# Kernel optimization log

Hardware: AMD Instinct MI355X
Metric: run time of the kernel (lower is better)

## Reference

```python
import jax, jax.numpy as jnp
import numpy as np

NUM_NODES = 50000
NUM_EDGES = 640000
IN_FEAT = 128
OUT_FEAT = 128


def setup_inputs() -> dict:
    key = jax.random.key(0)
    k1, k2, k3, k4 = jax.random.split(key, 4)
    features = jax.random.normal(k1, (NUM_NODES, IN_FEAT), dtype=jnp.float32)
    weight = jax.random.normal(k2, (IN_FEAT, OUT_FEAT), dtype=jnp.float32) * (1.0 / np.sqrt(IN_FEAT))
    edges_dst = jax.random.randint(k3, (NUM_EDGES,), 0, NUM_NODES, dtype=jnp.int32)
    edges_src = jax.random.randint(k4, (NUM_EDGES,), 0, NUM_NODES, dtype=jnp.int32)
    return {"features": features, "weight": weight, "edges_dst": edges_dst, "edges_src": edges_src}


def reference(features, weight, edges_dst, edges_src):
    # nodes_representation = features @ W   -> [N, out_feat]
    nodes_representation = jnp.matmul(features, weight)

    # gather neighbor (source) features: [E, in_feat]
    neighbour = features[edges_src]

    # unsorted_segment_mean over target node ids (edges_dst)
    seg_sum = jax.ops.segment_sum(neighbour, edges_dst, num_segments=NUM_NODES)
    counts = jax.ops.segment_sum(jnp.ones((NUM_EDGES,), dtype=features.dtype),
                                 edges_dst, num_segments=NUM_NODES)
    aggregated = jnp.where(counts[:, None] > 0, seg_sum / jnp.maximum(counts[:, None], 1.0), 0.0)

    aggregated_messages = jnp.matmul(aggregated, weight)  # [N, out_feat]

    # combination_type == 'concat', activation == 'relu'
    h = jnp.concatenate([nodes_representation, aggregated_messages], axis=-1)  # [N, 2*out_feat]
    return jax.nn.relu(h)
```

## Files before the change

### kernel.cpp

```cpp
#include <hip/hip_runtime.h>

#define FEAT 128
#define NPB 50
#define NB 1000
#define MAGIC50 85899346u
#define CELL 16
#define CAP 48
#define SBLK 256
#define SB_STRIDE 136

typedef __attribute__((ext_vector_type(8))) short bhalf8;
typedef __attribute__((ext_vector_type(4))) float floatx4;

__device__ __forceinline__ unsigned int cvtpk(float lo, float hi) {
    unsigned int r;
    asm("v_cvt_pk_bf16_f32 %0, %1, %2" : "=v"(r) : "v"(lo), "v"(hi));
    return r;
}

__device__ __forceinline__ void acc8(float* a, uint4 v) {
    a[0] += __uint_as_float(v.x << 16);
    a[1] += __uint_as_float(v.x & 0xffff0000u);
    a[2] += __uint_as_float(v.y << 16);
    a[3] += __uint_as_float(v.y & 0xffff0000u);
    a[4] += __uint_as_float(v.z << 16);
    a[5] += __uint_as_float(v.z & 0xffff0000u);
    a[6] += __uint_as_float(v.w << 16);
    a[7] += __uint_as_float(v.w & 0xffff0000u);
}

__global__ __launch_bounds__(256, 2) void fused_kernel(
    const float* __restrict__ feat, const float* __restrict__ W,
    unsigned short* __restrict__ P2, float* __restrict__ out, int nrows,
    const int* __restrict__ edst, const int* __restrict__ esrc,
    unsigned int* __restrict__ binned, int nE)
{
    __shared__ __align__(16) char smem[NB * CELL * 4 + (NB / 4) * 4];

    const int tid = threadIdx.x;

    if (blockIdx.x < SBLK) {
        unsigned int* lbin  = (unsigned int*)smem;
        unsigned int* cur32 = (unsigned int*)(smem + NB * CELL * 4);

        const int blk = blockIdx.x;
        for (int i = tid; i < NB / 4; i += 256) cur32[i] = 0u;
        __syncthreads();

        const int nE4 = nE >> 2;
        const int perBlk = (nE4 + SBLK - 1) / SBLK;
        const int gBeg = blk * perBlk;
        const int gEnd = min(gBeg + perBlk, nE4);

        for (int g = gBeg + tid; g < gEnd; g += 256) {
            int4 d = *(const int4*)&edst[g << 2];
            int4 s = *(const int4*)&esrc[g << 2];
            #pragma unroll
            for (int e = 0; e < 4; ++e) {
                int dd = (e == 0) ? d.x : (e == 1) ? d.y : (e == 2) ? d.z : d.w;
                int ss = (e == 0) ? s.x : (e == 1) ? s.y : (e == 2) ? s.z : s.w;
                unsigned int bin = __umulhi((unsigned int)dd, MAGIC50);
                int local = dd - (int)bin * NPB;
                const int sh = (bin & 3) * 8;
                unsigned int old = atomicAdd(&cur32[bin >> 2], 1u << sh);
                int slot = (int)((old >> sh) & 0xffu);
                if (slot < CELL - 1)
                    lbin[bin * CELL + 1 + slot] =
                        ((unsigned int)local << 16) | (unsigned int)(ss & 0xffff);
            }
        }
        if (blk == 0) {
            for (int i = (nE4 << 2) + tid; i < nE; i += 256) {
                int dd = edst[i], ss = esrc[i];
                unsigned int bin = __umulhi((unsigned int)dd, MAGIC50);
                int local = dd - (int)bin * NPB;
                const int sh = (bin & 3) * 8;
                unsigned int old = atomicAdd(&cur32[bin >> 2], 1u << sh);
                int slot = (int)((old >> sh) & 0xffu);
                if (slot < CELL - 1)
                    lbin[bin * CELL + 1 + slot] =
                        ((unsigned int)local << 16) | (unsigned int)(ss & 0xffff);
            }
        }
        __syncthreads();

        for (int bin = tid; bin < NB; bin += 256) {
            unsigned int c = (cur32[bin >> 2] >> ((bin & 3) * 8)) & 0xffu;
            lbin[bin * CELL] = min(c, (unsigned int)(CELL - 1));
        }
        __syncthreads();

        const int lane = tid & 63;
        const int wv   = tid >> 6;
        const int q    = lane & 3;
        for (int cg = wv * 16 + (lane >> 2); cg < NB; cg += 64) {
            uint4 v = *(const uint4*)&lbin[cg * CELL + q * 4];
            *(uint4*)&binned[((size_t)cg * SBLK + blk) * CELL + q * 4] = v;
        }
        return;
    }

    unsigned short* sB = (unsigned short*)smem;
    const int bx   = blockIdx.x - SBLK;
    const int wave = tid >> 6;
    const int lane = tid & 63;
    const int m    = lane & 15;
    const int kg   = lane >> 4;

    for (int i = tid; i < 2048; i += 256) {
        int n  = i & 127;
        int kc = i >> 7;
        const float* wp = &W[(size_t)(kc * 8) * FEAT + n];
        float f[8];
        #pragma unroll
        for (int t = 0; t < 8; ++t) f[t] = wp[(size_t)t * FEAT];
        uint4 p;
        p.x = cvtpk(f[0], f[1]);
        p.y = cvtpk(f[2], f[3]);
        p.z = cvtpk(f[4], f[5]);
        p.w = cvtpk(f[6], f[7]);
        *(uint4*)&sB[n * SB_STRIDE + kc * 8] = p;
    }

    const int row  = bx * 64 + wave * 16 + m;
    const int rowc = min(row, nrows - 1);
    bhalf8 afrag[4];
    {
        const float* ap = &feat[(size_t)rowc * FEAT + kg * 8];
        #pragma unroll
        for (int ks = 0; ks < 4; ++ks) {
            float4 f0 = *(const float4*)&ap[ks * 32];
            float4 f1 = *(const float4*)&ap[ks * 32 + 4];
            union { bhalf8 v; unsigned int u[4]; } a;
            a.u[0] = cvtpk(f0.x, f0.y);
            a.u[1] = cvtpk(f0.z, f0.w);
            a.u[2] = cvtpk(f1.x, f1.y);
            a.u[3] = cvtpk(f1.z, f1.w);
            afrag[ks] = a.v;
        }
    }

    __syncthreads();

    floatx4 acc[8];
    #pragma unroll
    for (int nt = 0; nt < 8; ++nt) acc[nt] = (floatx4){0.f, 0.f, 0.f, 0.f};

    #pragma unroll
    for (int ks = 0; ks < 4; ++ks) {
        #pragma unroll
        for (int nt = 0; nt < 8; ++nt) {
            bhalf8 b = *(bhalf8*)&sB[(nt * 16 + m) * SB_STRIDE + ks * 32 + kg * 8];
            acc[nt] = __builtin_amdgcn_mfma_f32_16x16x32_bf16(afrag[ks], b, acc[nt], 0, 0, 0);
        }
    }

    const int rbase = bx * 64 + wave * 16 + kg * 4;
    #pragma unroll
    for (int i = 0; i < 4; ++i) {
        int r = rbase + i;
        if (r < nrows) {
            #pragma unroll
            for (int nt = 0; nt < 8; nt += 2) {
                float v0 = acc[nt][i];
                float v1 = acc[nt + 1][i];
                int c = nt * 16 + m;
                out[(size_t)r * (2 * FEAT) + c]      = fmaxf(v0, 0.f);
                out[(size_t)r * (2 * FEAT) + c + 16] = fmaxf(v1, 0.f);
                unsigned int pk = cvtpk(v0, v1);
                P2[(size_t)r * FEAT + c]      = (unsigned short)(pk & 0xffffu);
                P2[(size_t)r * FEAT + c + 16] = (unsigned short)(pk >> 16);
            }
        }
    }
}

__global__ __launch_bounds__(256, 8) void aggregate_kernel(
    const unsigned short* __restrict__ P2, const unsigned int* __restrict__ binned,
    float* __restrict__ out, int n)
{
    __shared__ int lcnt[NPB];
    __shared__ unsigned short lbkt[NPB * CAP];

    const int bin = blockIdx.x;
    const int tid = threadIdx.x;

    for (int i = tid; i < NPB; i += 256) lcnt[i] = 0;
    __syncthreads();

    {
        const unsigned int* cell = &binned[((size_t)bin * SBLK + tid) * CELL];
        const int cnt = (int)cell[0];
        for (int k = 0; k < cnt; ++k) {
            unsigned int u = cell[1 + k];
            int local = (int)(u >> 16);
            int slot = atomicAdd(&lcnt[local], 1);
            if (slot < CAP) lbkt[local * CAP + slot] = (unsigned short)(u & 0xffffu);
        }
    }
    __syncthreads();

    const int qw = tid >> 4;
    const int cl = tid & 15;

    for (int l = qw; l < NPB; l += 16) {
        const int node = bin * NPB + l;
        if (node >= n) continue;
        const int deg = min(lcnt[l], CAP);

        float acc[8];
        #pragma unroll
        for (int t = 0; t < 8; ++t) acc[t] = 0.f;

        const unsigned short* bkt = &lbkt[l * CAP];
        for (int j0 = 0; j0 < deg; j0 += 4) {
            int s0 = (int)bkt[j0];
            int s1 = (j0 + 1 < deg) ? (int)bkt[j0 + 1] : s0;
            int s2 = (j0 + 2 < deg) ? (int)bkt[j0 + 2] : s0;
            int s3 = (j0 + 3 < deg) ? (int)bkt[j0 + 3] : s0;
            uint4 v0 = *(const uint4*)&P2[(size_t)s0 * FEAT + cl * 8];
            uint4 v1 = *(const uint4*)&P2[(size_t)s1 * FEAT + cl * 8];
            uint4 v2 = *(const uint4*)&P2[(size_t)s2 * FEAT + cl * 8];
            uint4 v3 = *(const uint4*)&P2[(size_t)s3 * FEAT + cl * 8];
            if (j0 + 1 >= deg) v1 = make_uint4(0u, 0u, 0u, 0u);
            if (j0 + 2 >= deg) v2 = make_uint4(0u, 0u, 0u, 0u);
            if (j0 + 3 >= deg) v3 = make_uint4(0u, 0u, 0u, 0u);
            acc8(acc, v0);
            acc8(acc, v1);
            acc8(acc, v2);
            acc8(acc, v3);
        }

        const float inv = (deg > 0) ? (1.0f / (float)deg) : 0.0f;
        float4 r0 = make_float4(fmaxf(acc[0] * inv, 0.f), fmaxf(acc[1] * inv, 0.f),
                                fmaxf(acc[2] * inv, 0.f), fmaxf(acc[3] * inv, 0.f));
        float4 r1 = make_float4(fmaxf(acc[4] * inv, 0.f), fmaxf(acc[5] * inv, 0.f),
                                fmaxf(acc[6] * inv, 0.f), fmaxf(acc[7] * inv, 0.f));
        float* op = &out[(size_t)node * (2 * FEAT) + FEAT + cl * 8];
        *(float4*)op = r0;
        *(float4*)(op + 4) = r1;
    }
}

extern "C" void kernel_launch(void* const* d_in, const int* in_sizes, int n_in,
                              void* d_out, int out_size, void* d_ws, size_t ws_size,
                              hipStream_t stream)
{
    const float* feat = (const float*)d_in[0];
    const float* W    = (const float*)d_in[1];
    const int* edst   = (const int*)d_in[2];
    const int* esrc   = (const int*)d_in[3];
    float* out        = (float*)d_out;

    const int N = in_sizes[0] / FEAT;
    const int E = in_sizes[2];

    char* ws = (char*)d_ws;
    unsigned short* P2 = (unsigned short*)ws;
    size_t off = (size_t)N * FEAT * sizeof(unsigned short);
    off = (off + 63) & ~(size_t)63;
    unsigned int* binned = (unsigned int*)(ws + off);
    off += (size_t)NB * SBLK * CELL * 4;

    const int gemmBlocks = (N + 63) / 64;
    fused_kernel<<<SBLK + gemmBlocks, 256, 0, stream>>>(
        feat, W, P2, out, N, edst, esrc, binned, E);

    aggregate_kernel<<<NB, 256, 0, stream>>>(P2, binned, out, N);
}
```

Before: 125.0 us.

## Split edge binning across two half-range blocks to shrink LDS and raise occupancy

Each binning block now handles only half of the destination bins (500 instead of 1000), and twice as many binning blocks are launched. Each one reads its full edge slice and drops edges that fall outside its half. This roughly halves the LDS footprint, so launch bounds move from 2 to 4 blocks per CU for the fused binning/GEMM kernel. The trade-off is that every edge index array is read twice and twice as many blocks run the filter checks.

```diff
diff --git a/kernel.cpp b/kernel.cpp
--- a/kernel.cpp
+++ b/kernel.cpp
@@ -3,6 +3,7 @@
 #define FEAT 128
 #define NPB 50
 #define NB 1000
+#define HB 500
 #define MAGIC50 85899346u
 #define CELL 16
 #define CAP 48
@@ -29,22 +30,26 @@
     a[7] += __uint_as_float(v.w & 0xffff0000u);
 }
 
-__global__ __launch_bounds__(256, 2) void fused_kernel(
+__global__ __launch_bounds__(256, 4) void fused_kernel(
     const float* __restrict__ feat, const float* __restrict__ W,
     unsigned short* __restrict__ P2, float* __restrict__ out, int nrows,
     const int* __restrict__ edst, const int* __restrict__ esrc,
     unsigned int* __restrict__ binned, int nE)
 {
-    __shared__ __align__(16) char smem[NB * CELL * 4 + (NB / 4) * 4];
+    __shared__ __align__(16) char smem[128 * SB_STRIDE * 2];
 
     const int tid = threadIdx.x;
 
-    if (blockIdx.x < SBLK) {
+    if (blockIdx.x < 2 * SBLK) {
         unsigned int* lbin  = (unsigned int*)smem;
-        unsigned int* cur32 = (unsigned int*)(smem + NB * CELL * 4);
-
-        const int blk = blockIdx.x;
-        for (int i = tid; i < NB / 4; i += 256) cur32[i] = 0u;
+        unsigned int* cur32 = (unsigned int*)(smem + HB * CELL * 4);
+
+        const int sb   = blockIdx.x;
+        const int blk  = sb & (SBLK - 1);
+        const int half = sb >> 8;
+        const unsigned int binBase = half * HB;
+
+        for (int i = tid; i < HB / 4; i += 256) cur32[i] = 0u;
         __syncthreads();
 
         const int nE4 = nE >> 2;
@@ -60,48 +65,54 @@
                 int dd = (e == 0) ? d.x : (e == 1) ? d.y : (e == 2) ? d.z : d.w;
                 int ss = (e == 0) ? s.x : (e == 1) ? s.y : (e == 2) ? s.z : s.w;
                 unsigned int bin = __umulhi((unsigned int)dd, MAGIC50);
-                int local = dd - (int)bin * NPB;
-                const int sh = (bin & 3) * 8;
-                unsigned int old = atomicAdd(&cur32[bin >> 2], 1u << sh);
-                int slot = (int)((old >> sh) & 0xffu);
-                if (slot < CELL - 1)
-                    lbin[bin * CELL + 1 + slot] =
-                        ((unsigned int)local << 16) | (unsigned int)(ss & 0xffff);
+                unsigned int lb = bin - binBase;
+                if (lb < HB) {
+                    int local = dd - (int)bin * NPB;
+                    const int sh = (lb & 3) * 8;
+                    unsigned int old = atomicAdd(&cur32[lb >> 2], 1u << sh);
+                    int slot = (int)((old >> sh) & 0xffu);
+                    if (slot < CELL - 1)
+                        lbin[lb * CELL + 1 + slot] =
+                            ((unsigned int)local << 16) | (unsigned int)(ss & 0xffff);
+                }
             }
         }
         if (blk == 0) {
             for (int i = (nE4 << 2) + tid; i < nE; i += 256) {
                 int dd = edst[i], ss = esrc[i];
                 unsigned int bin = __umulhi((unsigned int)dd, MAGIC50);
-                int local = dd - (int)bin * NPB;
-                const int sh = (bin & 3) * 8;
-                unsigned int old = atomicAdd(&cur32[bin >> 2], 1u << sh);
-                int slot = (int)((old >> sh) & 0xffu);
-                if (slot < CELL - 1)
-                    lbin[bin * CELL + 1 + slot] =
-                        ((unsigned int)local << 16) | (unsigned int)(ss & 0xffff);
+                unsigned int lb = bin - binBase;
+                if (lb < HB) {
+                    int local = dd - (int)bin * NPB;
+                    const int sh = (lb & 3) * 8;
+                    unsigned int old = atomicAdd(&cur32[lb >> 2], 1u << sh);
+                    int slot = (int)((old >> sh) & 0xffu);
+                    if (slot < CELL - 1)
+                        lbin[lb * CELL + 1 + slot] =
+                            ((unsigned int)local << 16) | (unsigned int)(ss & 0xffff);
+                }
             }
         }
         __syncthreads();
 
-        for (int bin = tid; bin < NB; bin += 256) {
-            unsigned int c = (cur32[bin >> 2] >> ((bin & 3) * 8)) & 0xffu;
-            lbin[bin * CELL] = min(c, (unsigned int)(CELL - 1));
+        for (int lb = tid; lb < HB; lb += 256) {
+            unsigned int c = (cur32[lb >> 2] >> ((lb & 3) * 8)) & 0xffu;
+            lbin[lb * CELL] = min(c, (unsigned int)(CELL - 1));
         }
         __syncthreads();
 
         const int lane = tid & 63;
         const int wv   = tid >> 6;
         const int q    = lane & 3;
-        for (int cg = wv * 16 + (lane >> 2); cg < NB; cg += 64) {
+        for (int cg = wv * 16 + (lane >> 2); cg < HB; cg += 64) {
             uint4 v = *(const uint4*)&lbin[cg * CELL + q * 4];
-            *(uint4*)&binned[((size_t)cg * SBLK + blk) * CELL + q * 4] = v;
+            *(uint4*)&binned[((size_t)(binBase + cg) * SBLK + blk) * CELL + q * 4] = v;
         }
         return;
     }
 
     unsigned short* sB = (unsigned short*)smem;
-    const int bx   = blockIdx.x - SBLK;
+    const int bx   = blockIdx.x - 2 * SBLK;
     const int wave = tid >> 6;
     const int lane = tid & 63;
     const int m    = lane & 15;
@@ -263,7 +274,7 @@
     off += (size_t)NB * SBLK * CELL * 4;
 
     const int gemmBlocks = (N + 63) / 64;
-    fused_kernel<<<SBLK + gemmBlocks, 256, 0, stream>>>(
+    fused_kernel<<<2 * SBLK + gemmBlocks, 256, 0, stream>>>(
         feat, W, P2, out, N, edst, esrc, binned, E);
 
     aggregate_kernel<<<NB, 256, 0, stream>>>(P2, binned, out, N);
```

After: 127.8 us. 2.2% more time.
